# Kernel optimization log

Hardware: AMD Instinct MI355X
Metric: run time of the kernel (lower is better)

## Reference

```python
import jax, jax.numpy as jnp
import numpy as np

N = 100000      # nodes
DEG = 16        # avg degree
E = N * DEG     # edges
D = 128         # feature dim
U = 128         # output units


def setup_inputs() -> dict:
    key = jax.random.key(0)
    k1, k2, k3, k4 = jax.random.split(key, 4)
    node_features = jax.random.normal(k1, (N, D), dtype=jnp.float32)
    # every row has exactly DEG entries so the 'mean' combiner never divides by zero
    edge_rows = jnp.arange(E, dtype=jnp.int64) // DEG
    edge_cols = jax.random.randint(k2, (E,), 0, N, dtype=jnp.int64)
    edge_weights = jax.random.uniform(k3, (E,), dtype=jnp.float32, minval=0.1, maxval=1.0)
    W = jax.random.normal(k4, (D, U), dtype=jnp.float32) * (1.0 / np.sqrt(D))
    b = jnp.zeros((U,), dtype=jnp.float32)
    return {"node_features": node_features, "edge_rows": edge_rows,
            "edge_cols": edge_cols, "edge_weights": edge_weights, "W": W, "b": b}


def reference(node_features, edge_rows, edge_cols, edge_weights, W, b):
    # embedding_lookup_sparse_v2 with combiner='mean':
    # agg[i] = sum_j w_ij * feat[j] / sum_j w_ij
    gathered = node_features[edge_cols] * edge_weights[:, None]   # [E, D]
    num = jax.ops.segment_sum(gathered, edge_rows, num_segments=N)  # [N, D]
    den = jax.ops.segment_sum(edge_weights, edge_rows, num_segments=N)  # [N]
    agg = num / den[:, None]
    # Dense(units, activation='relu'); dropout/l2_norm are built but not applied in call()
    return jax.nn.relu(agg @ W + b)
```

## Files before the change

### kernel.cpp

```cpp
#include <hip/hip_runtime.h>

#define N_NODES 100000
#define DEG 16
#define D_DIM 128
#define U_DIM 128
#define FSTRIDE 136

typedef __bf16 bf16x8 __attribute__((ext_vector_type(8)));
typedef float f32x4 __attribute__((ext_vector_type(4)));
typedef unsigned int u32x4 __attribute__((ext_vector_type(4)));

__device__ __forceinline__ unsigned short f2bf(float x) {
    unsigned int u = __float_as_uint(x);
    u += 0x7fffu + ((u >> 16) & 1u);
    return (unsigned short)(u >> 16);
}
__device__ __forceinline__ unsigned int pack2(float a, float b) {
    return (unsigned int)f2bf(a) | ((unsigned int)f2bf(b) << 16);
}

__global__ void cast_w_kernel(const float* __restrict__ W,
                              unsigned short* __restrict__ WT) {
    int t = blockIdx.x * 256 + threadIdx.x;
    int k = t >> 7, n = t & 127;
    WT[n * 128 + k] = f2bf(W[t]);
}

__global__ __launch_bounds__(256)
void ymat_kernel(const float* __restrict__ feat,
                 const unsigned short* __restrict__ WT,
                 const float* __restrict__ bias,
                 unsigned short* __restrict__ Y) {
    __shared__ __align__(16) unsigned short ftile[128 * FSTRIDE];
    const int lane = threadIdx.x & 63;
    const int wv = threadIdx.x >> 6;
    const int quad = lane >> 4;
    const int l15 = lane & 15;
    const int n0 = blockIdx.x * 128;
    const int u_base = wv * 32;

    {
        const int t = threadIdx.x;
        #pragma unroll
        for (int j = 0; j < 16; ++j) {
            const int i = j * 256 + t;
            const int row = i >> 5;
            const int col = (i & 31) * 4;
            const int rowc = (n0 + row < N_NODES) ? (n0 + row) : (N_NODES - 1);
            const float4 v = *(const float4*)(feat + (size_t)rowc * D_DIM + col);
            ushort4 s;
            s.x = f2bf(v.x); s.y = f2bf(v.y); s.z = f2bf(v.z); s.w = f2bf(v.w);
            *(ushort4*)&ftile[row * FSTRIDE + col] = s;
        }
    }

    bf16x8 afr[2][4];
    #pragma unroll
    for (int ni = 0; ni < 2; ++ni) {
        const int u = u_base + ni * 16 + l15;
        #pragma unroll
        for (int kc = 0; kc < 4; ++kc)
            afr[ni][kc] = *(const bf16x8*)(WT + u * 128 + kc * 32 + quad * 8);
    }
    const float4 bv0 = *(const float4*)(bias + u_base + quad * 4);
    const float4 bv1 = *(const float4*)(bias + u_base + 16 + quad * 4);

    __syncthreads();

    #pragma unroll
    for (int mi = 0; mi < 8; ++mi) {
        const int node = n0 + mi * 16 + l15;
        bf16x8 bfr[4];
        #pragma unroll
        for (int kc = 0; kc < 4; ++kc)
            bfr[kc] = *(const bf16x8*)&ftile[(mi * 16 + l15) * FSTRIDE + kc * 32 + quad * 8];
        f32x4 acc0 = (f32x4){0.f, 0.f, 0.f, 0.f};
        f32x4 acc1 = (f32x4){0.f, 0.f, 0.f, 0.f};
        #pragma unroll
        for (int kc = 0; kc < 4; ++kc) {
            acc0 = __builtin_amdgcn_mfma_f32_16x16x32_bf16(afr[0][kc], bfr[kc], acc0, 0, 0, 0);
            acc1 = __builtin_amdgcn_mfma_f32_16x16x32_bf16(afr[1][kc], bfr[kc], acc1, 0, 0, 0);
        }
        if (node < N_NODES) {
            unsigned int* yp = (unsigned int*)(Y + (size_t)node * U_DIM + u_base + quad * 4);
            uint2 s0, s1;
            s0.x = pack2(acc0[0] + bv0.x, acc0[1] + bv0.y);
            s0.y = pack2(acc0[2] + bv0.z, acc0[3] + bv0.w);
            s1.x = pack2(acc1[0] + bv1.x, acc1[1] + bv1.y);
            s1.y = pack2(acc1[2] + bv1.z, acc1[3] + bv1.w);
            *(uint2*)yp = s0;
            *(uint2*)(yp + 8) = s1;
        }
    }
}

__global__ __launch_bounds__(256, 4)
void agg_kernel(const unsigned short* __restrict__ Y,
                const int* __restrict__ cols,
                const float* __restrict__ wts,
                float* __restrict__ out) {
    const int phase = (blockIdx.x >= 3125) ? 1 : 0;
    const int nb = blockIdx.x - phase * 3125;
    const int node = nb * 32 + (threadIdx.x >> 3);
    const int ubase = phase * 64 + (threadIdx.x & 7) * 8;
    const int e0 = node * DEG;

    int cc[DEG];
    float ww[DEG];
    #pragma unroll
    for (int q = 0; q < 4; ++q) {
        const int4 c4 = *(const int4*)(cols + e0 + 4 * q);
        const float4 w4 = *(const float4*)(wts + e0 + 4 * q);
        cc[4 * q + 0] = c4.x; cc[4 * q + 1] = c4.y;
        cc[4 * q + 2] = c4.z; cc[4 * q + 3] = c4.w;
        ww[4 * q + 0] = w4.x; ww[4 * q + 1] = w4.y;
        ww[4 * q + 2] = w4.z; ww[4 * q + 3] = w4.w;
    }
    float den = 0.f;
    #pragma unroll
    for (int e = 0; e < DEG; ++e) den += ww[e];

    const unsigned short* ybase = Y + ubase;
    u32x4 p[DEG];
    #pragma unroll
    for (int e = 0; e < DEG; ++e) {
        const unsigned long long a =
            (unsigned long long)(ybase + (size_t)cc[e] * U_DIM);
        asm volatile("global_load_dwordx4 %0, %1, off" : "=v"(p[e]) : "v"(a));
    }
    asm volatile("s_waitcnt vmcnt(0)" ::: "memory");
    __builtin_amdgcn_sched_barrier(0);

    float a0 = 0.f, a1 = 0.f, a2 = 0.f, a3 = 0.f;
    float a4 = 0.f, a5 = 0.f, a6 = 0.f, a7 = 0.f;
    #pragma unroll
    for (int e = 0; e < DEG; ++e) {
        const float w = ww[e];
        a0 = fmaf(w, __uint_as_float(p[e][0] << 16), a0);
        a1 = fmaf(w, __uint_as_float(p[e][0] & 0xffff0000u), a1);
        a2 = fmaf(w, __uint_as_float(p[e][1] << 16), a2);
        a3 = fmaf(w, __uint_as_float(p[e][1] & 0xffff0000u), a3);
        a4 = fmaf(w, __uint_as_float(p[e][2] << 16), a4);
        a5 = fmaf(w, __uint_as_float(p[e][2] & 0xffff0000u), a5);
        a6 = fmaf(w, __uint_as_float(p[e][3] << 16), a6);
        a7 = fmaf(w, __uint_as_float(p[e][3] & 0xffff0000u), a7);
    }
    const float inv = 1.0f / den;
    f32x4 o0, o1;
    o0[0] = fmaxf(a0 * inv, 0.f); o0[1] = fmaxf(a1 * inv, 0.f);
    o0[2] = fmaxf(a2 * inv, 0.f); o0[3] = fmaxf(a3 * inv, 0.f);
    o1[0] = fmaxf(a4 * inv, 0.f); o1[1] = fmaxf(a5 * inv, 0.f);
    o1[2] = fmaxf(a6 * inv, 0.f); o1[3] = fmaxf(a7 * inv, 0.f);
    f32x4* op = (f32x4*)(out + (size_t)node * U_DIM + ubase);
    __builtin_nontemporal_store(o0, op);
    __builtin_nontemporal_store(o1, op + 1);
}

extern "C" void kernel_launch(void* const* d_in, const int* in_sizes, int n_in,
                              void* d_out, int out_size, void* d_ws, size_t ws_size,
                              hipStream_t stream) {
    const float* feat = (const float*)d_in[0];
    const int* cols  = (const int*)d_in[2];
    const float* wts = (const float*)d_in[3];
    const float* W   = (const float*)d_in[4];
    const float* b   = (const float*)d_in[5];
    float* out = (float*)d_out;

    unsigned short* wt_bf = (unsigned short*)d_ws;
    unsigned short* Y     = (unsigned short*)((char*)d_ws + 32768);

    cast_w_kernel<<<16384 / 256, 256, 0, stream>>>(W, wt_bf);

    const int nblocks = (N_NODES + 127) / 128;
    ymat_kernel<<<nblocks, 256, 0, stream>>>(feat, wt_bf, b, Y);

    agg_kernel<<<6250, 256, 0, stream>>>(Y, cols, wts, out);
}
```

Before: 176.2 us.

## Load features directly into MFMA registers, dropping the LDS staging tile

The Y = feat·W kernel stops staging a 128-node fp32→bf16 tile in shared memory. Each block now handles 16 nodes, and every lane loads its own feature row fragment straight from global memory into registers, converting it to a bf16 MFMA operand. This removes the LDS writes, the barrier and the LDS reads, and launches 8x more blocks to raise occupancy. In exchange, each block re-reads the bf16 weight fragments for only 16 nodes, and the feature loads are less coalesced, since each lane does strided 16B loads and the four waves load the same rows.

```diff
diff --git a/kernel.cpp b/kernel.cpp
--- a/kernel.cpp
+++ b/kernel.cpp
@@ -4,7 +4,6 @@
 #define DEG 16
 #define D_DIM 128
 #define U_DIM 128
-#define FSTRIDE 136
 
 typedef __bf16 bf16x8 __attribute__((ext_vector_type(8)));
 typedef float f32x4 __attribute__((ext_vector_type(4)));
@@ -26,32 +25,24 @@
     WT[n * 128 + k] = f2bf(W[t]);
 }
 
-__global__ __launch_bounds__(256)
+__global__ __launch_bounds__(256, 4)
 void ymat_kernel(const float* __restrict__ feat,
                  const unsigned short* __restrict__ WT,
                  const float* __restrict__ bias,
                  unsigned short* __restrict__ Y) {
-    __shared__ __align__(16) unsigned short ftile[128 * FSTRIDE];
     const int lane = threadIdx.x & 63;
     const int wv = threadIdx.x >> 6;
     const int quad = lane >> 4;
     const int l15 = lane & 15;
-    const int n0 = blockIdx.x * 128;
+    const int node = blockIdx.x * 16 + l15;
     const int u_base = wv * 32;
 
-    {
-        const int t = threadIdx.x;
-        #pragma unroll
-        for (int j = 0; j < 16; ++j) {
-            const int i = j * 256 + t;
-            const int row = i >> 5;
-            const int col = (i & 31) * 4;
-            const int rowc = (n0 + row < N_NODES) ? (n0 + row) : (N_NODES - 1);
-            const float4 v = *(const float4*)(feat + (size_t)rowc * D_DIM + col);
-            ushort4 s;
-            s.x = f2bf(v.x); s.y = f2bf(v.y); s.z = f2bf(v.z); s.w = f2bf(v.w);
-            *(ushort4*)&ftile[row * FSTRIDE + col] = s;
-        }
+    const float* frow = feat + (size_t)node * D_DIM;
+    float4 f0[4], f1[4];
+    #pragma unroll
+    for (int kc = 0; kc < 4; ++kc) {
+        f0[kc] = *(const float4*)(frow + kc * 32 + quad * 8);
+        f1[kc] = *(const float4*)(frow + kc * 32 + quad * 8 + 4);
     }
 
     bf16x8 afr[2][4];
@@ -65,33 +56,33 @@
     const float4 bv0 = *(const float4*)(bias + u_base + quad * 4);
     const float4 bv1 = *(const float4*)(bias + u_base + 16 + quad * 4);
 
-    __syncthreads();
+    bf16x8 bfr[4];
+    #pragma unroll
+    for (int kc = 0; kc < 4; ++kc) {
+        u32x4 t;
+        t[0] = pack2(f0[kc].x, f0[kc].y);
+        t[1] = pack2(f0[kc].z, f0[kc].w);
+        t[2] = pack2(f1[kc].x, f1[kc].y);
+        t[3] = pack2(f1[kc].z, f1[kc].w);
+        bfr[kc] = __builtin_bit_cast(bf16x8, t);
+    }
 
+    f32x4 acc0 = (f32x4){0.f, 0.f, 0.f, 0.f};
+    f32x4 acc1 = (f32x4){0.f, 0.f, 0.f, 0.f};
     #pragma unroll
-    for (int mi = 0; mi < 8; ++mi) {
-        const int node = n0 + mi * 16 + l15;
-        bf16x8 bfr[4];
-        #pragma unroll
-        for (int kc = 0; kc < 4; ++kc)
-            bfr[kc] = *(const bf16x8*)&ftile[(mi * 16 + l15) * FSTRIDE + kc * 32 + quad * 8];
-        f32x4 acc0 = (f32x4){0.f, 0.f, 0.f, 0.f};
-        f32x4 acc1 = (f32x4){0.f, 0.f, 0.f, 0.f};
-        #pragma unroll
-        for (int kc = 0; kc < 4; ++kc) {
-            acc0 = __builtin_amdgcn_mfma_f32_16x16x32_bf16(afr[0][kc], bfr[kc], acc0, 0, 0, 0);
-            acc1 = __builtin_amdgcn_mfma_f32_16x16x32_bf16(afr[1][kc], bfr[kc], acc1, 0, 0, 0);
-        }
-        if (node < N_NODES) {
-            unsigned int* yp = (unsigned int*)(Y + (size_t)node * U_DIM + u_base + quad * 4);
-            uint2 s0, s1;
-            s0.x = pack2(acc0[0] + bv0.x, acc0[1] + bv0.y);
-            s0.y = pack2(acc0[2] + bv0.z, acc0[3] + bv0.w);
-            s1.x = pack2(acc1[0] + bv1.x, acc1[1] + bv1.y);
-            s1.y = pack2(acc1[2] + bv1.z, acc1[3] + bv1.w);
-            *(uint2*)yp = s0;
-            *(uint2*)(yp + 8) = s1;
-        }
+    for (int kc = 0; kc < 4; ++kc) {
+        acc0 = __builtin_amdgcn_mfma_f32_16x16x32_bf16(afr[0][kc], bfr[kc], acc0, 0, 0, 0);
+        acc1 = __builtin_amdgcn_mfma_f32_16x16x32_bf16(afr[1][kc], bfr[kc], acc1, 0, 0, 0);
     }
+
+    unsigned int* yp = (unsigned int*)(Y + (size_t)node * U_DIM + u_base + quad * 4);
+    uint2 s0, s1;
+    s0.x = pack2(acc0[0] + bv0.x, acc0[1] + bv0.y);
+    s0.y = pack2(acc0[2] + bv0.z, acc0[3] + bv0.w);
+    s1.x = pack2(acc1[0] + bv1.x, acc1[1] + bv1.y);
+    s1.y = pack2(acc1[2] + bv1.z, acc1[3] + bv1.w);
+    *(uint2*)yp = s0;
+    *(uint2*)(yp + 8) = s1;
 }
 
 __global__ __launch_bounds__(256, 4)
@@ -171,8 +162,7 @@
 
     cast_w_kernel<<<16384 / 256, 256, 0, stream>>>(W, wt_bf);
 
-    const int nblocks = (N_NODES + 127) / 128;
-    ymat_kernel<<<nblocks, 256, 0, stream>>>(feat, wt_bf, b, Y);
+    ymat_kernel<<<N_NODES / 16, 256, 0, stream>>>(feat, wt_bf, b, Y);
 
     agg_kernel<<<6250, 256, 0, stream>>>(Y, cols, wts, out);
 }
```

Measured after the change: 203.5 us. 1.15x slower.
